# Performance work log

Measured on AMD Instinct MI355X. Metric: run time of the kernel, lower is better.

Reference implementation:

```python
import jax, jax.numpy as jnp
import numpy as np

DIM = 768
H = 12          # num query heads
KV = 6          # num kv heads
GS = H // KV    # group size = 2
HD = DIM // H   # head dim = 64


def setup_inputs() -> dict:
    key = jax.random.key(0)
    ks = jax.random.split(key, 6)
    B, P = 8, 1024
    s = DIM ** -0.5
    x = jax.random.normal(ks[0], (B, P, DIM), dtype=jnp.float32)
    Wq = jax.random.normal(ks[1], (DIM, DIM), dtype=jnp.float32) * s
    Wk = jax.random.normal(ks[2], (DIM, KV * HD), dtype=jnp.float32) * s
    Wv = jax.random.normal(ks[3], (DIM, KV * HD), dtype=jnp.float32) * s
    Wp = jax.random.normal(ks[4], (DIM, DIM), dtype=jnp.float32) * s
    bp = jnp.zeros((DIM,), dtype=jnp.float32)
    return {"x": x, "Wq": Wq, "Wk": Wk, "Wv": Wv, "Wp": Wp, "bp": bp}


def reference(x, Wq, Wk, Wv, Wp, bp):
    B, P, C = x.shape
    scale = HD ** -0.5
    # projections; consecutive heads i*GS..(i+1)*GS-1 form kv-group i (torch.split dim=1)
    q = (x @ Wq).reshape(B, P, KV, GS, HD).transpose(0, 2, 3, 1, 4) * scale  # [B,KV,GS,P,d]
    k = (x @ Wk).reshape(B, P, KV, HD).transpose(0, 2, 1, 3)                 # [B,KV,P,d]
    v = (x @ Wv).reshape(B, P, KV, HD).transpose(0, 2, 1, 3)                 # [B,KV,P,d]

    scores = jnp.einsum('bghqd,bgkd->bghqk', q, k)      # [B,KV,GS,P,P]
    w = jax.nn.softmax(scores, axis=-1)                  # attn_drop=0 (eval)
    att = jnp.einsum('bghqk,bgkd->bghqd', w, v)          # [B,KV,GS,P,d]

    # per-group row-matched gaussian-ish noise (torch get_gaussian), vectorized over KV groups
    y = P * HD
    flat = att.reshape(B, KV, GS, y)                     # rows = groups within kv-group
    M = jax.random.uniform(jax.random.key(42), (KV, GS, y), dtype=flat.dtype)
    di = jnp.arange(min(GS, y))
    M = M.at[:, di, di].set(0.0)                         # sparse: zero diagonal
    m_mean = M.mean(axis=-1, keepdims=True)
    m_std = jnp.std(M, axis=-1, ddof=1, keepdims=True)   # torch.std is unbiased
    m_std = jnp.where(m_std == 0, jnp.ones_like(m_std), m_std)
    Z = (M - m_mean) / m_std                             # [KV,GS,y], shared across batch
    r_mean = flat.mean(axis=-1, keepdims=True)           # [B,KV,GS,1]
    r_std = jnp.std(flat, axis=-1, ddof=1, keepdims=True)
    flat = flat - (Z[None] * r_std + r_mean)

    att = flat.reshape(B, KV, GS, P, HD).reshape(B, H, P, HD)
    out = att.transpose(0, 2, 1, 3).reshape(B, P, C) @ Wp + bp  # proj_drop=0
    return out
```

## Files before the change

kernel.cpp:

```cpp
#include <hip/hip_runtime.h>
#include <hip/hip_bf16.h>
#include <math.h>


#define NTHREADS 256

typedef __bf16 bf16x8 __attribute__((ext_vector_type(8)));
typedef float f32x4 __attribute__((ext_vector_type(4)));

#define MFMA16(a, b, c) __builtin_amdgcn_mfma_f32_16x16x32_bf16(a, b, c, 0, 0, 0)

#define QSCALE 0.18033688011112042f

__device__ __forceinline__ float fexp2(float x) {
#if __has_builtin(__builtin_amdgcn_exp2f)
    return __builtin_amdgcn_exp2f(x);
#else
    return __expf(x * 0.6931471805599453f);
#endif
}

__device__ __forceinline__ void gload16(const void* g, void* l) {
    __builtin_amdgcn_global_load_lds(
        (const __attribute__((address_space(1))) void*)g,
        (__attribute__((address_space(3))) void*)l, 16, 0, 0);
}

__device__ __forceinline__ unsigned rotl_u32(unsigned x, int r) {
    return (x << r) | (x >> (32 - r));
}
__device__ __forceinline__ void threefry_0_42(unsigned x0, unsigned x1,
                                              unsigned& o0, unsigned& o1) {
    const unsigned ks0 = 0u, ks1 = 42u, ks2 = 0u ^ 42u ^ 0x1BD11BDAu;
    x0 += ks0; x1 += ks1;
#define R4(a,b,c,d) \
    x0 += x1; x1 = rotl_u32(x1,a); x1 ^= x0; \
    x0 += x1; x1 = rotl_u32(x1,b); x1 ^= x0; \
    x0 += x1; x1 = rotl_u32(x1,c); x1 ^= x0; \
    x0 += x1; x1 = rotl_u32(x1,d); x1 ^= x0;
    R4(13,15,26,6)   x0 += ks1; x1 += ks2 + 1u;
    R4(17,29,16,24)  x0 += ks2; x1 += ks0 + 2u;
    R4(13,15,26,6)   x0 += ks0; x1 += ks1 + 3u;
    R4(17,29,16,24)  x0 += ks1; x1 += ks2 + 4u;
    R4(13,15,26,6)   x0 += ks2; x1 += ks0 + 5u;
#undef R4
    o0 = x0; o1 = x1;
}
__device__ __forceinline__ float tf_uniform(unsigned i) {
    unsigned o0, o1;
    threefry_0_42(0u, i, o0, o1);
    unsigned bits = o0 ^ o1;
    return __uint_as_float((bits >> 9) | 0x3f800000u) - 1.0f;
}

__device__ __forceinline__ float wave_sum64(float v) {
#pragma unroll
    for (int off = 32; off; off >>= 1) v += __shfl_xor(v, off, 64);
    return v;
}

__device__ __forceinline__ unsigned short bf16_rne(float x) {
    unsigned u = __float_as_uint(x);
    return (unsigned short)((u + 0x7fffu + ((u >> 16) & 1u)) >> 16);
}
__device__ __forceinline__ unsigned pack_bf16x2(float lo, float hi) {
    return (unsigned)bf16_rne(lo) | ((unsigned)bf16_rne(hi) << 16);
}
__device__ __forceinline__ float bfu(unsigned v) {
    return __uint_as_float(v << 16);
}

__global__ __launch_bounds__(NTHREADS) void prep_k(
    const float* __restrict__ x, const float* __restrict__ Wq,
    const float* __restrict__ Wk, const float* __restrict__ Wv,
    const float* __restrict__ Wp,
    unsigned short* __restrict__ xb, unsigned short* __restrict__ wqt,
    unsigned short* __restrict__ wkt, unsigned short* __restrict__ wvt,
    unsigned short* __restrict__ wpt,
    unsigned short* __restrict__ zb, float* __restrict__ zpart)
{
    __shared__ float rbuf[8];
    int blk = blockIdx.x;
    if (blk < 1536) {
#pragma unroll
        for (int j = 0; j < 4; ++j) {
            int i = blk * 1024 + j * 256 + threadIdx.x;
            float4 v = ((const float4*)x)[i];
            uint2 u;
            u.x = pack_bf16x2(v.x, v.y);
            u.y = pack_bf16x2(v.z, v.w);
            *(uint2*)(xb + (size_t)i * 4) = u;
        }
    } else if (blk < 1920) {
        int zc = blk - 1536;
        int row = zc >> 5, chunk = zc & 31;
        int g = row & 1;
        int j0 = chunk * 2048;
        float sum = 0.f, sumsq = 0.f;
        for (int t = threadIdx.x; t < 2048; t += NTHREADS) {
            int j = j0 + t;
            unsigned i = (unsigned)row * 65536u + (unsigned)j;
            float m = tf_uniform(i);
            if (j == g) m = 0.f;
            zb[i] = bf16_rne(m);
            sum += m; sumsq += m * m;
        }
        sum = wave_sum64(sum); sumsq = wave_sum64(sumsq);
        int lane = threadIdx.x & 63, wv = threadIdx.x >> 6;
        if (lane == 0) { rbuf[wv] = sum; rbuf[4 + wv] = sumsq; }
        __syncthreads();
        if (threadIdx.x == 0) {
            zpart[zc * 2]     = rbuf[0] + rbuf[1] + rbuf[2] + rbuf[3];
            zpart[zc * 2 + 1] = rbuf[4] + rbuf[5] + rbuf[6] + rbuf[7];
        }
    } else {
        int id = blk - 1920;
        const float* W; unsigned short* Wt; int N;
        if (id < 144)      { W = Wq; Wt = wqt; N = 768; }
        else if (id < 216) { W = Wk; Wt = wkt; N = 384; id -= 144; }
        else if (id < 288) { W = Wv; Wt = wvt; N = 384; id -= 216; }
        else               { W = Wp; Wt = wpt; N = 768; id -= 288; }
        int ntn = N >> 6;
        int kt = id / ntn, nt = id % ntn;
        int k0 = kt * 64, n0 = nt * 64;
        int t = threadIdx.x;
        int tn = t & 63, tk = t >> 6;
        float r[16];
#pragma unroll
        for (int j = 0; j < 16; ++j)
            r[j] = W[(size_t)(k0 + tk * 16 + j) * N + n0 + tn];
        uint4 u0, u1;
        u0.x = pack_bf16x2(r[0], r[1]);   u0.y = pack_bf16x2(r[2], r[3]);
        u0.z = pack_bf16x2(r[4], r[5]);   u0.w = pack_bf16x2(r[6], r[7]);
        u1.x = pack_bf16x2(r[8], r[9]);   u1.y = pack_bf16x2(r[10], r[11]);
        u1.z = pack_bf16x2(r[12], r[13]); u1.w = pack_bf16x2(r[14], r[15]);
        unsigned short* dst = Wt + (size_t)(n0 + tn) * 768 + k0 + tk * 16;
        *(uint4*)dst = u0;
        *(uint4*)(dst + 8) = u1;
    }
}

__device__ __forceinline__ void mfma_tile128x256(
    const unsigned short* __restrict__ A, const unsigned short* __restrict__ Bt,
    int row0, int col0,
    unsigned short* As, unsigned short* Bs, f32x4 acc[4][4])
{
    const int tid = threadIdx.x;
    const int w = tid >> 6, lane = tid & 63;
    const int c = lane & 15, g = lane >> 4;
    const int wm = w & 1, wn = w >> 1;

#pragma unroll
    for (int mi = 0; mi < 4; ++mi)
#pragma unroll
        for (int ni = 0; ni < 4; ++ni) acc[mi][ni] = (f32x4){0.f, 0.f, 0.f, 0.f};

    const unsigned short* gsrc[6];
    unsigned short* ldst[6];
#pragma unroll
    for (int j = 0; j < 6; ++j) {
        int seg = w * 6 + j;
        bool isA = seg < 16;
        int s = isA ? seg : seg - 16;
        int chunk = s >> 1, kh = s & 1;
        const unsigned short* gb = isA
            ? (A  + (size_t)(row0 + chunk * 16 + c) * 768)
            : (Bt + (size_t)(col0 + chunk * 16 + c) * 768);
        gsrc[j] = gb + kh * 32 + g * 8;
        ldst[j] = (isA ? As : Bs) + chunk * 1024 + kh * 512 + lane * 8;
    }

    for (int k0 = 0; k0 < 768; k0 += 64) {
        __syncthreads();
#pragma unroll
        for (int j = 0; j < 6; ++j) gload16(gsrc[j] + k0, ldst[j]);
        __syncthreads();
#pragma unroll
        for (int ks = 0; ks < 2; ++ks) {
            bf16x8 aA[4], bB[4];
#pragma unroll
            for (int mi = 0; mi < 4; ++mi)
                aA[mi] = *(const bf16x8*)&As[(wm * 4 + mi) * 1024 + ks * 512 + g * 128 + c * 8];
#pragma unroll
            for (int ni = 0; ni < 4; ++ni)
                bB[ni] = *(const bf16x8*)&Bs[(wn * 4 + ni) * 1024 + ks * 512 + g * 128 + c * 8];
#pragma unroll
            for (int mi = 0; mi < 4; ++mi)
#pragma unroll
                for (int ni = 0; ni < 4; ++ni)
                    acc[mi][ni] = MFMA16(aA[mi], bB[ni], acc[mi][ni]);
        }
    }
}

__global__ __launch_bounds__(512) void qkv_mfma_k(
    const unsigned short* __restrict__ xb, const unsigned short* __restrict__ wstk,
    unsigned short* __restrict__ qbh, unsigned short* __restrict__ kb2,
    unsigned short* __restrict__ vb2)
{
    __shared__ unsigned short As[8192];
    __shared__ unsigned short Bs[16384];
    int id = blockIdx.x;
    int xcd = id & 7, slot = id >> 3;
    int col0i = xcd + ((slot & 3) << 3);
    int row0i = slot >> 2;
    int row0 = row0i * 128, col0 = col0i * 256;
    f32x4 acc[4][4];
    mfma_tile128x256(wstk, xb, row0, col0, As, Bs, acc);

    const int tid = threadIdx.x;
    const int w = tid >> 6, lane = tid & 63;
    const int c = lane & 15, g = lane >> 4;
    const int wm = w & 1, wn = w >> 1;

#pragma unroll
    for (int mi = 0; mi < 4; ++mi) {
        int ocb = row0 + wm * 64 + mi * 16;
        int ocol = ocb + g * 4;
#pragma unroll
        for (int ni = 0; ni < 4; ++ni) {
            int pglob = col0 + wn * 64 + ni * 16 + c;
            int b = pglob >> 10, pin = pglob & 1023;
            if (ocb < 768) {
                ushort4 u;
                u.x = bf16_rne(acc[mi][ni][0] * QSCALE);
                u.y = bf16_rne(acc[mi][ni][1] * QSCALE);
                u.z = bf16_rne(acc[mi][ni][2] * QSCALE);
                u.w = bf16_rne(acc[mi][ni][3] * QSCALE);
                int h = ocol >> 6, d0 = ocol & 63;
                *(ushort4*)&qbh[(((size_t)b * 12 + h) * 1024 + pin) * 64 + d0] = u;
            } else if (ocb < 1152) {
                int kcol = ocol - 768;
                int kv = kcol >> 6, d0 = kcol & 63;
                int kt = pin >> 7, key = pin & 127;
                ushort4 u;
                u.x = bf16_rne(acc[mi][ni][0]);
                u.y = bf16_rne(acc[mi][ni][1]);
                u.z = bf16_rne(acc[mi][ni][2]);
                u.w = bf16_rne(acc[mi][ni][3]);
                *(ushort4*)&kb2[((((size_t)(b * 6 + kv) * 8 + kt) * 8 + (d0 >> 3)) * 128
                                 + key) * 8 + (d0 & 7)] = u;
            } else {
                int kt = pin >> 7, pg = (pin & 127) >> 3, p8 = pin & 7;
#pragma unroll
                for (int r = 0; r < 4; ++r) {
                    int vcol = ocol + r - 1152;
                    int kv = vcol >> 6, d = vcol & 63;
                    vb2[((((size_t)(b * 6 + kv) * 8 + kt) * 16 + pg) * 64 + d) * 8 + p8]
                        = bf16_rne(acc[mi][ni][r]);
                }
            }
        }
    }
}

__global__ __launch_bounds__(512) void proj_mfma_k(
    const unsigned short* __restrict__ attb, const unsigned short* __restrict__ wpt,
    const float* __restrict__ bp, float* __restrict__ out)
{
    __shared__ unsigned short As[8192];
    __shared__ unsigned short Bs[16384];
    int id = blockIdx.x;
    int xcd = id & 7, slot = id >> 3;
    int col0i = xcd + ((slot & 3) << 3);
    int row0i = slot >> 2;
    int row0 = row0i * 128, col0 = col0i * 256;
    f32x4 acc[4][4];
    mfma_tile128x256(wpt, attb, row0, col0, As, Bs, acc);

    const int tid = threadIdx.x;
    const int w = tid >> 6, lane = tid & 63;
    const int c = lane & 15, g = lane >> 4;
    const int wm = w & 1, wn = w >> 1;
#pragma unroll
    for (int mi = 0; mi < 4; ++mi) {
        int ocol = row0 + wm * 64 + mi * 16 + g * 4;
        float4 bias = *(const float4*)&bp[ocol];
#pragma unroll
        for (int ni = 0; ni < 4; ++ni) {
            int p = col0 + wn * 64 + ni * 16 + c;
            float4 u;
            u.x = acc[mi][ni][0] + bias.x;
            u.y = acc[mi][ni][1] + bias.y;
            u.z = acc[mi][ni][2] + bias.z;
            u.w = acc[mi][ni][3] + bias.w;
            *(float4*)&out[(size_t)p * 768 + ocol] = u;
        }
    }
}

#define LDP 136
__global__ __launch_bounds__(NTHREADS) void attn_mfma_k(
    const unsigned short* __restrict__ qbh, const unsigned short* __restrict__ kb2,
    const unsigned short* __restrict__ vb2, unsigned short* __restrict__ attb,
    float* __restrict__ spart)
{
    __shared__ unsigned short P_lds[4 * 32 * LDP];
    __shared__ float l_s[4][32];
    __shared__ float sbuf[8];

    int id = blockIdx.x;
    int xcd = id & 7, slot = id >> 3;
    int grp = slot % 6, member = slot / 6;
    int g48 = xcd + 8 * grp;
    int b = g48 / 6, kv = g48 % 6;
    int h = kv * 2 + (member & 1);
    int qtile = member >> 1;
    const int qt0 = qtile * 128;

    const int tid = threadIdx.x;
    const int w = tid >> 6, lane = tid & 63;
    const int c = lane & 15, g = lane >> 4;

    const unsigned short* qh = qbh + (((size_t)b * 12 + h) * 1024 + qt0 + w * 32) * 64;
    const unsigned short* kbase = kb2 + ((size_t)(b * 6 + kv) * 8) * 8192;
    const unsigned short* vbase = vb2 + ((size_t)(b * 6 + kv) * 8) * 8192;
    unsigned short* Pw = P_lds + w * 32 * LDP;

    bf16x8 bQ[2][2];
#pragma unroll
    for (int ks = 0; ks < 2; ++ks) {
        bQ[ks][0] = *(const bf16x8*)(qh + (size_t)(c) * 64 + ks * 32 + g * 8);
        bQ[ks][1] = *(const bf16x8*)(qh + (size_t)(16 + c) * 64 + ks * 32 + g * 8);
    }

    f32x4 O[2][4];
#pragma unroll
    for (int i = 0; i < 2; ++i)
#pragma unroll
        for (int j = 0; j < 4; ++j) O[i][j] = (f32x4){0.f, 0.f, 0.f, 0.f};
    float l_r[2] = {0.f, 0.f};

    for (int t = 0; t < 8; ++t) {
        const unsigned short* kt = kbase + (size_t)t * 8192;
        const unsigned short* vt = vbase + (size_t)t * 8192;

        bf16x8 aK[2][8];
#pragma unroll
        for (int ks = 0; ks < 2; ++ks)
#pragma unroll
            for (int mb = 0; mb < 8; ++mb)
                aK[ks][mb] = *(const bf16x8*)(kt + ((size_t)(ks * 4 + g) * 128 + mb * 16 + c) * 8);

        f32x4 S[8][2];
#pragma unroll
        for (int mb = 0; mb < 8; ++mb) {
            S[mb][0] = (f32x4){0.f, 0.f, 0.f, 0.f};
            S[mb][1] = (f32x4){0.f, 0.f, 0.f, 0.f};
        }
#pragma unroll
        for (int ks = 0; ks < 2; ++ks)
#pragma unroll
            for (int mb = 0; mb < 8; ++mb) {
                S[mb][0] = MFMA16(aK[ks][mb], bQ[ks][0], S[mb][0]);
                S[mb][1] = MFMA16(aK[ks][mb], bQ[ks][1], S[mb][1]);
            }

        bf16x8 bV[4][4];
#pragma unroll
        for (int ks = 0; ks < 4; ++ks)
#pragma unroll
            for (int nb = 0; nb < 4; ++nb)
                bV[ks][nb] = *(const bf16x8*)(vt + ((size_t)(ks * 4 + g) * 64 + nb * 16 + c) * 8);

#pragma unroll
        for (int qn = 0; qn < 2; ++qn) {
            float lt = 0.f;
#pragma unroll
            for (int mb = 0; mb < 8; ++mb) {
                float p0 = fexp2(S[mb][qn][0]);
                float p1 = fexp2(S[mb][qn][1]);
                float p2 = fexp2(S[mb][qn][2]);
                float p3 = fexp2(S[mb][qn][3]);
                lt += (p0 + p1) + (p2 + p3);
                uint2 uu;
                uu.x = pack_bf16x2(p0, p1);
                uu.y = pack_bf16x2(p2, p3);
                *(uint2*)&Pw[(size_t)(qn * 16 + c) * LDP + mb * 16 + g * 4] = uu;
            }
            lt += __shfl_xor(lt, 16, 64);
            lt += __shfl_xor(lt, 32, 64);
            l_r[qn] += lt;
        }

#pragma unroll
        for (int ks = 0; ks < 4; ++ks) {
            bf16x8 aP0 = *(const bf16x8*)&Pw[(size_t)(c) * LDP + ks * 32 + g * 8];
            bf16x8 aP1 = *(const bf16x8*)&Pw[(size_t)(16 + c) * LDP + ks * 32 + g * 8];
#pragma unroll
            for (int nb = 0; nb < 4; ++nb) {
                O[0][nb] = MFMA16(aP0, bV[ks][nb], O[0][nb]);
                O[1][nb] = MFMA16(aP1, bV[ks][nb], O[1][nb]);
            }
        }
    }
    if (g == 0) { l_s[w][c] = l_r[0]; l_s[w][16 + c] = l_r[1]; }
    f32x4 li0 = *(f32x4*)&l_s[w][g * 4];
    f32x4 li1 = *(f32x4*)&l_s[w][16 + g * 4];
    float inv0[4], inv1[4];
#pragma unroll
    for (int r = 0; r < 4; ++r) { inv0[r] = 1.f / li0[r]; inv1[r] = 1.f / li1[r]; }
    unsigned short* ob = attb + ((size_t)b * 1024 + qt0 + w * 32) * 768 + h * 64;
    float psum = 0.f, psumsq = 0.f;
#pragma unroll
    for (int r = 0; r < 4; ++r) {
#pragma unroll
        for (int nb = 0; nb < 4; ++nb) {
            float o0 = O[0][nb][r] * inv0[r];
            float o1 = O[1][nb][r] * inv1[r];
            psum += o0 + o1;
            psumsq += o0 * o0 + o1 * o1;
            ob[(size_t)(g * 4 + r) * 768 + nb * 16 + c]      = bf16_rne(o0);
            ob[(size_t)(16 + g * 4 + r) * 768 + nb * 16 + c] = bf16_rne(o1);
        }
    }
    psum = wave_sum64(psum); psumsq = wave_sum64(psumsq);
    if (lane == 0) { sbuf[w] = psum; sbuf[4 + w] = psumsq; }
    __syncthreads();
    if (tid == 0) {
        int idx = ((b * 12 + h) * 8 + qtile) * 2;
        spart[idx]     = sbuf[0] + sbuf[1] + sbuf[2] + sbuf[3];
        spart[idx + 1] = sbuf[4] + sbuf[5] + sbuf[6] + sbuf[7];
    }
}

__global__ __launch_bounds__(NTHREADS) void stats2_k(
    unsigned short* __restrict__ attb, const unsigned short* __restrict__ zb,
    const float* __restrict__ spart, const float* __restrict__ zpart)
{
    int blk = blockIdx.x;
    int bh = blk >> 3, ch = blk & 7;
    int b = bh / 12, h = bh % 12;
    float zs = 0.f, zs2 = 0.f, rs = 0.f, rs2 = 0.f;
#pragma unroll
    for (int cc = 0; cc < 32; ++cc) {
        zs  += zpart[(h * 32 + cc) * 2];
        zs2 += zpart[(h * 32 + cc) * 2 + 1];
    }
#pragma unroll
    for (int cc = 0; cc < 8; ++cc) {
        rs  += spart[(bh * 8 + cc) * 2];
        rs2 += spart[(bh * 8 + cc) * 2 + 1];
    }
    float m_mean = zs * (1.f / 65536.f);
    float m_var  = (zs2 - 65536.f * m_mean * m_mean) * (1.f / 65535.f);
    float m_sd   = sqrtf(fmaxf(m_var, 0.f));
    if (m_sd == 0.f) m_sd = 1.f;
    float r_mean = rs * (1.f / 65536.f);
    float r_var  = (rs2 - 65536.f * r_mean * r_mean) * (1.f / 65535.f);
    float r_sd   = sqrtf(fmaxf(r_var, 0.f));
    float a = r_sd / m_sd;
    float bc = m_mean * a - r_mean;

    unsigned short* base = attb + ((size_t)b * 1024 + ch * 128) * 768 + h * 64;
    const unsigned short* zrow = zb + (size_t)h * 65536 + (size_t)ch * 8192;
    for (int f = threadIdx.x; f < 1024; f += NTHREADS) {
        int p = f >> 3, dq = (f & 7) * 8;
        unsigned short* ptr = base + (size_t)p * 768 + dq;
        uint4 u = *(const uint4*)ptr;
        uint4 zu = *(const uint4*)(zrow + (size_t)f * 8);
        float v0 = bfu(u.x)       - bfu(zu.x)       * a + bc;
        float v1 = bfu(u.x >> 16) - bfu(zu.x >> 16) * a + bc;
        float v2 = bfu(u.y)       - bfu(zu.y)       * a + bc;
        float v3 = bfu(u.y >> 16) - bfu(zu.y >> 16) * a + bc;
        float v4 = bfu(u.z)       - bfu(zu.z)       * a + bc;
        float v5 = bfu(u.z >> 16) - bfu(zu.z >> 16) * a + bc;
        float v6 = bfu(u.w)       - bfu(zu.w)       * a + bc;
        float v7 = bfu(u.w >> 16) - bfu(zu.w >> 16) * a + bc;
        uint4 o;
        o.x = pack_bf16x2(v0, v1);
        o.y = pack_bf16x2(v2, v3);
        o.z = pack_bf16x2(v4, v5);
        o.w = pack_bf16x2(v6, v7);
        *(uint4*)ptr = o;
    }
}

extern "C" void kernel_launch(void* const* d_in, const int* in_sizes, int n_in,
                              void* d_out, int out_size, void* d_ws, size_t ws_size,
                              hipStream_t stream) {
    const float* x  = (const float*)d_in[0];
    const float* Wq = (const float*)d_in[1];
    const float* Wk = (const float*)d_in[2];
    const float* Wv = (const float*)d_in[3];
    const float* Wp = (const float*)d_in[4];
    const float* bp = (const float*)d_in[5];
    float* out = (float*)d_out;

    float* ws    = (float*)d_ws;
    float* zpart = ws;
    float* spart = zpart + 768;
    unsigned short* zb   = (unsigned short*)(spart + 1536);
    unsigned short* xb   = zb + 786432;
    unsigned short* wqt  = xb + 6291456;
    unsigned short* wkt  = wqt + 589824;
    unsigned short* wvt  = wkt + 294912;
    unsigned short* wpt  = wvt + 294912;
    unsigned short* qbh  = wpt + 589824;
    unsigned short* kb2  = qbh + 6291456;
    unsigned short* vb2  = kb2 + 3145728;
    unsigned short* attb = vb2 + 3145728;

    prep_k<<<2352, NTHREADS, 0, stream>>>(x, Wq, Wk, Wv, Wp,
                                          xb, wqt, wkt, wvt, wpt, zb, zpart);
    qkv_mfma_k<<<384, 512, 0, stream>>>(xb, wqt, qbh, kb2, vb2);
    attn_mfma_k<<<768, NTHREADS, 0, stream>>>(qbh, kb2, vb2, attb, spart);
    stats2_k<<<768, NTHREADS, 0, stream>>>(attb, zb, spart, zpart);
    proj_mfma_k<<<192, 512, 0, stream>>>(attb, wpt, bp, out);
}
```

Before: 230.4 us.

## Store GEMM operands in pre-tiled fragment layout for contiguous LDS loads

The producers (prep_k, the attention epilogue and stats2_k) now write x, the weights and the attention output directly in a blocked layout that matches the LDS tile order used by the MFMA GEMMs. Each k-chunk tile then becomes one contiguous block, so the GEMM inner loop loads it with simple linear global-to-LDS copies instead of strided row gathers. The cost is scattered 2-byte stores in the attention epilogue and more index arithmetic in the producers.

New measurement: 188.7 us. 1.22x faster.

```diff
diff --git a/kernel.cpp b/kernel.cpp
--- a/kernel.cpp
+++ b/kernel.cpp
@@ -70,12 +70,12 @@
     return __uint_as_float(v << 16);
 }
 
+
 __global__ __launch_bounds__(NTHREADS) void prep_k(
     const float* __restrict__ x, const float* __restrict__ Wq,
     const float* __restrict__ Wk, const float* __restrict__ Wv,
     const float* __restrict__ Wp,
-    unsigned short* __restrict__ xb, unsigned short* __restrict__ wqt,
-    unsigned short* __restrict__ wkt, unsigned short* __restrict__ wvt,
+    unsigned short* __restrict__ xb, unsigned short* __restrict__ wstk,
     unsigned short* __restrict__ wpt,
     unsigned short* __restrict__ zb, float* __restrict__ zpart)
 {
@@ -89,7 +89,14 @@
             uint2 u;
             u.x = pack_bf16x2(v.x, v.y);
             u.y = pack_bf16x2(v.z, v.w);
-            *(uint2*)(xb + (size_t)i * 4) = u;
+            int f0 = i * 4;
+            int row = f0 / 768, col = f0 - row * 768;
+            int kc = col >> 6, kin = col & 63;
+            int kh = kin >> 5, g = (kin >> 3) & 3, e = col & 7;
+            int chunk = row >> 4, cl = row & 15;
+            size_t a = (((size_t)(kc * 512 + chunk)) * 2 + kh) * 512
+                       + (g * 16 + cl) * 8 + e;
+            *(uint2*)&xb[a] = u;
         }
     } else if (blk < 1920) {
         int zc = blk - 1536;
@@ -115,11 +122,11 @@
         }
     } else {
         int id = blk - 1920;
-        const float* W; unsigned short* Wt; int N;
-        if (id < 144)      { W = Wq; Wt = wqt; N = 768; }
-        else if (id < 216) { W = Wk; Wt = wkt; N = 384; id -= 144; }
-        else if (id < 288) { W = Wv; Wt = wvt; N = 384; id -= 216; }
-        else               { W = Wp; Wt = wpt; N = 768; id -= 288; }
+        const float* W; unsigned short* dstbuf; int N, rowbase, NC;
+        if (id < 144)      { W = Wq; dstbuf = wstk; N = 768; rowbase = 0;    NC = 96; }
+        else if (id < 216) { W = Wk; dstbuf = wstk; N = 384; rowbase = 768;  NC = 96; id -= 144; }
+        else if (id < 288) { W = Wv; dstbuf = wstk; N = 384; rowbase = 1152; NC = 96; id -= 216; }
+        else               { W = Wp; dstbuf = wpt;  N = 768; rowbase = 0;    NC = 48; id -= 288; }
         int ntn = N >> 6;
         int kt = id / ntn, nt = id % ntn;
         int k0 = kt * 64, n0 = nt * 64;
@@ -134,19 +141,24 @@
         u0.z = pack_bf16x2(r[4], r[5]);   u0.w = pack_bf16x2(r[6], r[7]);
         u1.x = pack_bf16x2(r[8], r[9]);   u1.y = pack_bf16x2(r[10], r[11]);
         u1.z = pack_bf16x2(r[12], r[13]); u1.w = pack_bf16x2(r[14], r[15]);
-        unsigned short* dst = Wt + (size_t)(n0 + tn) * 768 + k0 + tk * 16;
-        *(uint4*)dst = u0;
-        *(uint4*)(dst + 8) = u1;
+        int rowg = rowbase + n0 + tn;
+        int chunk = rowg >> 4, cl = rowg & 15;
+        int kc = k0 >> 6;
+        int kh = tk >> 1, g0 = (tk & 1) * 2;
+        size_t base = (((size_t)(kc * NC + chunk)) * 2 + kh) * 512 + cl * 8;
+        *(uint4*)&dstbuf[base + g0 * 128]       = u0;
+        *(uint4*)&dstbuf[base + (g0 + 1) * 128] = u1;
     }
 }
 
 __device__ __forceinline__ void mfma_tile128x256(
-    const unsigned short* __restrict__ A, const unsigned short* __restrict__ Bt,
+    const unsigned short* __restrict__ Afb, int nca,
+    const unsigned short* __restrict__ Bfb,
     int row0, int col0,
     unsigned short* As, unsigned short* Bs, f32x4 acc[4][4])
 {
     const int tid = threadIdx.x;
-    const int w = tid >> 6, lane = tid & 63;
+    const int lane = tid & 63, w = tid >> 6;
     const int c = lane & 15, g = lane >> 4;
     const int wm = w & 1, wn = w >> 1;
 
@@ -155,25 +167,19 @@
 #pragma unroll
         for (int ni = 0; ni < 4; ++ni) acc[mi][ni] = (f32x4){0.f, 0.f, 0.f, 0.f};
 
-    const unsigned short* gsrc[6];
-    unsigned short* ldst[6];
-#pragma unroll
-    for (int j = 0; j < 6; ++j) {
-        int seg = w * 6 + j;
-        bool isA = seg < 16;
-        int s = isA ? seg : seg - 16;
-        int chunk = s >> 1, kh = s & 1;
-        const unsigned short* gb = isA
-            ? (A  + (size_t)(row0 + chunk * 16 + c) * 768)
-            : (Bt + (size_t)(col0 + chunk * 16 + c) * 768);
-        gsrc[j] = gb + kh * 32 + g * 8;
-        ldst[j] = (isA ? As : Bs) + chunk * 1024 + kh * 512 + lane * 8;
-    }
-
-    for (int k0 = 0; k0 < 768; k0 += 64) {
+    const unsigned short* Abase = Afb + (size_t)(row0 >> 4) * 1024;
+    const unsigned short* Bbase = Bfb + (size_t)(col0 >> 4) * 1024;
+
+    for (int kc = 0; kc < 12; ++kc) {
+        const unsigned short* a = Abase + (size_t)kc * nca * 1024;
+        const unsigned short* bb = Bbase + (size_t)kc * 512 * 1024;
         __syncthreads();
-#pragma unroll
-        for (int j = 0; j < 6; ++j) gload16(gsrc[j] + k0, ldst[j]);
+        gload16(a  + tid * 8,         As + tid * 8);
+        gload16(a  + tid * 8 + 4096,  As + tid * 8 + 4096);
+        gload16(bb + tid * 8,         Bs + tid * 8);
+        gload16(bb + tid * 8 + 4096,  Bs + tid * 8 + 4096);
+        gload16(bb + tid * 8 + 8192,  Bs + tid * 8 + 8192);
+        gload16(bb + tid * 8 + 12288, Bs + tid * 8 + 12288);
         __syncthreads();
 #pragma unroll
         for (int ks = 0; ks < 2; ++ks) {
@@ -206,7 +212,7 @@
     int row0i = slot >> 2;
     int row0 = row0i * 128, col0 = col0i * 256;
     f32x4 acc[4][4];
-    mfma_tile128x256(wstk, xb, row0, col0, As, Bs, acc);
+    mfma_tile128x256(wstk, 96, xb, row0, col0, As, Bs, acc);
 
     const int tid = threadIdx.x;
     const int w = tid >> 6, lane = tid & 63;
@@ -266,7 +272,7 @@
     int row0i = slot >> 2;
     int row0 = row0i * 128, col0 = col0i * 256;
     f32x4 acc[4][4];
-    mfma_tile128x256(wpt, attb, row0, col0, As, Bs, acc);
+    mfma_tile128x256(wpt, 48, attb, row0, col0, As, Bs, acc);
 
     const int tid = threadIdx.x;
     const int w = tid >> 6, lane = tid & 63;
@@ -400,18 +406,24 @@
     float inv0[4], inv1[4];
 #pragma unroll
     for (int r = 0; r < 4; ++r) { inv0[r] = 1.f / li0[r]; inv1[r] = 1.f / li1[r]; }
-    unsigned short* ob = attb + ((size_t)b * 1024 + qt0 + w * 32) * 768 + h * 64;
+    int rowblk = (b * 1024 + qt0 + w * 32) >> 4;
     float psum = 0.f, psumsq = 0.f;
 #pragma unroll
     for (int r = 0; r < 4; ++r) {
+        int cl = g * 4 + r;
 #pragma unroll
         for (int nb = 0; nb < 4; ++nb) {
             float o0 = O[0][nb][r] * inv0[r];
             float o1 = O[1][nb][r] * inv1[r];
             psum += o0 + o1;
             psumsq += o0 * o0 + o1 * o1;
-            ob[(size_t)(g * 4 + r) * 768 + nb * 16 + c]      = bf16_rne(o0);
-            ob[(size_t)(16 + g * 4 + r) * 768 + nb * 16 + c] = bf16_rne(o1);
+            int kh = nb >> 1, gb = (nb & 1) * 2 + (c >> 3), e = c & 7;
+            size_t a0 = (((size_t)h * 512 + rowblk) * 2 + kh) * 512
+                        + (gb * 16 + cl) * 8 + e;
+            size_t a1 = (((size_t)h * 512 + rowblk + 1) * 2 + kh) * 512
+                        + (gb * 16 + cl) * 8 + e;
+            attb[a0] = bf16_rne(o0);
+            attb[a1] = bf16_rne(o1);
         }
     }
     psum = wave_sum64(psum); psumsq = wave_sum64(psumsq);
@@ -452,11 +464,14 @@
     float a = r_sd / m_sd;
     float bc = m_mean * a - r_mean;
 
-    unsigned short* base = attb + ((size_t)b * 1024 + ch * 128) * 768 + h * 64;
     const unsigned short* zrow = zb + (size_t)h * 65536 + (size_t)ch * 8192;
     for (int f = threadIdx.x; f < 1024; f += NTHREADS) {
         int p = f >> 3, dq = (f & 7) * 8;
-        unsigned short* ptr = base + (size_t)p * 768 + dq;
+        int row = b * 1024 + ch * 128 + p;
+        int chunk = row >> 4, cl = row & 15;
+        int kh = dq >> 5, gb = (dq >> 3) & 3;
+        size_t aoff = (((size_t)h * 512 + chunk) * 2 + kh) * 512 + (gb * 16 + cl) * 8;
+        unsigned short* ptr = attb + aoff;
         uint4 u = *(const uint4*)ptr;
         uint4 zu = *(const uint4*)(zrow + (size_t)f * 8);
         float v0 = bfu(u.x)       - bfu(zu.x)       * a + bc;
@@ -492,18 +507,16 @@
     float* spart = zpart + 768;
     unsigned short* zb   = (unsigned short*)(spart + 1536);
     unsigned short* xb   = zb + 786432;
-    unsigned short* wqt  = xb + 6291456;
-    unsigned short* wkt  = wqt + 589824;
-    unsigned short* wvt  = wkt + 294912;
-    unsigned short* wpt  = wvt + 294912;
+    unsigned short* wstk = xb + 6291456;
+    unsigned short* wpt  = wstk + 1179648;
     unsigned short* qbh  = wpt + 589824;
     unsigned short* kb2  = qbh + 6291456;
     unsigned short* vb2  = kb2 + 3145728;
     unsigned short* attb = vb2 + 3145728;
 
     prep_k<<<2352, NTHREADS, 0, stream>>>(x, Wq, Wk, Wv, Wp,
-                                          xb, wqt, wkt, wvt, wpt, zb, zpart);
-    qkv_mfma_k<<<384, 512, 0, stream>>>(xb, wqt, qbh, kb2, vb2);
+                                          xb, wstk, wpt, zb, zpart);
+    qkv_mfma_k<<<384, 512, 0, stream>>>(xb, wstk, qbh, kb2, vb2);
     attn_mfma_k<<<768, NTHREADS, 0, stream>>>(qbh, kb2, vb2, attb, spart);
     stats2_k<<<768, NTHREADS, 0, stream>>>(attb, zb, spart, zpart);
     proj_mfma_k<<<192, 512, 0, stream>>>(attb, wpt, bp, out);
```
